# Optimization experiments

Measured on AMD Instinct MI355X. Metric: run time of the kernel, lower is better.

## Reference

```python
import jax, jax.numpy as jnp
import numpy as np

N_NODES = 50000
GRAPH_DIM = 256
QUERY_DIM = 256
BATCH = 512


def setup_inputs() -> dict:
    key = jax.random.key(0)
    k1, k2, k3 = jax.random.split(key, 3)
    graph_embs = jax.random.normal(k1, (N_NODES, GRAPH_DIM), dtype=jnp.float32)
    query_emb = jax.random.normal(k2, (BATCH, QUERY_DIM), dtype=jnp.float32)
    # nn.Linear(graph_dim + query_dim, 1): weight [1, G+Q] -> stored flat [G+Q], bias [1]
    attn_w = jax.random.normal(k3, (GRAPH_DIM + QUERY_DIM,), dtype=jnp.float32) * (1.0 / np.sqrt(GRAPH_DIM + QUERY_DIM))
    attn_b = jnp.zeros((1,), dtype=jnp.float32)
    return {"graph_embs": graph_embs, "query_emb": query_emb, "attn_w": attn_w, "attn_b": attn_b}


def reference(graph_embs, query_emb, attn_w, attn_b):
    # Linear on concat([graph, query]) == graph @ w_g + query @ w_q + b
    w_g = attn_w[:GRAPH_DIM]   # [G]
    w_q = attn_w[GRAPH_DIM:]   # [Q]
    g_score = graph_embs @ w_g            # [N]
    q_score = query_emb @ w_q             # [B]
    scores = q_score[:, None] + g_score[None, :] + attn_b[0]  # [B, N]
    attn_weights = jax.nn.softmax(scores, axis=-1)            # [B, N]
    pooled = attn_weights @ graph_embs                        # [B, G]
    return pooled
```

## Files before the change

### kernel.cpp

```cpp
#include <hip/hip_runtime.h>


#define N_NODES 50000
#define DIM     256
#define BATCH   512
#define CHUNK   50
#define GRID1   1000
#define NPART   8
#define POISON  0xAAAAAAAAu

__global__ __launch_bounds__(256) void qap_fused(
    const float* __restrict__ embs,
    const float* __restrict__ attn_w,
    float* __restrict__ part,
    float* __restrict__ zpart,
    unsigned int* __restrict__ counter,
    float* __restrict__ out)
{
    __shared__ float accLDS[4][DIM];
    __shared__ float zWave[4];
    __shared__ int   isLast;
    const int tid  = threadIdx.x;
    const int wave = tid >> 6;
    const int lane = tid & 63;
    const int beg  = blockIdx.x * CHUNK;
    const int rep  = blockIdx.x & (NPART - 1);

    const float4* emb4 = (const float4*)embs;
    const float4  w    = ((const float4*)attn_w)[lane];

    float4 acc  = {0.f, 0.f, 0.f, 0.f};
    float  zAcc = 0.f;

    for (int i = wave * 2; i < CHUNK; i += 8) {
        const float4 v0 = emb4[(size_t)(beg + i) * 64 + lane];
        const float4 v1 = emb4[(size_t)(beg + i + 1) * 64 + lane];
        float p0 = v0.x * w.x + v0.y * w.y + v0.z * w.z + v0.w * w.w;
        float p1 = v1.x * w.x + v1.y * w.y + v1.z * w.z + v1.w * w.w;
        #pragma unroll
        for (int off = 32; off >= 1; off >>= 1) {
            p0 += __shfl_xor(p0, off, 64);
            p1 += __shfl_xor(p1, off, 64);
        }
        const float e0 = __expf(p0);
        const float e1 = __expf(p1);
        zAcc += e0 + e1;
        acc.x = fmaf(e0, v0.x, fmaf(e1, v1.x, acc.x));
        acc.y = fmaf(e0, v0.y, fmaf(e1, v1.y, acc.y));
        acc.z = fmaf(e0, v0.z, fmaf(e1, v1.z, acc.z));
        acc.w = fmaf(e0, v0.w, fmaf(e1, v1.w, acc.w));
    }

    ((float4*)&accLDS[wave][0])[lane] = acc;
    if (lane == 0) zWave[wave] = zAcc;
    __syncthreads();
    const float s = accLDS[0][tid] + accLDS[1][tid] + accLDS[2][tid] + accLDS[3][tid];
    atomicAdd(&part[rep * DIM + tid], s);
    if (tid == 0)
        atomicAdd(&zpart[rep], zWave[0] + zWave[1] + zWave[2] + zWave[3]);

    __builtin_amdgcn_s_waitcnt(0);
    __syncthreads();
    if (tid == 0) {
        const unsigned int old = atomicAdd(counter, 1u);
        isLast = (old == POISON + (GRID1 - 1u)) || (old == GRID1 - 1u);
    }
    __syncthreads();
    if (!isLast) return;

    float sv = 0.f;
    #pragma unroll
    for (int j = 0; j < NPART; ++j)
        sv += __hip_atomic_load(&part[j * DIM + tid],
                                __ATOMIC_RELAXED, __HIP_MEMORY_SCOPE_AGENT);
    float z = 0.f;
    if (tid == 0) {
        #pragma unroll
        for (int j = 0; j < NPART; ++j)
            z += __hip_atomic_load(&zpart[j],
                                   __ATOMIC_RELAXED, __HIP_MEMORY_SCOPE_AGENT);
    }
    __shared__ float zsh;
    if (tid == 0) zsh = z;
    __shared__ float outv[DIM];
    __syncthreads();
    outv[tid] = sv * (1.0f / zsh);
    __syncthreads();

    const float4 o = ((const float4*)outv)[lane];
    float4* out4 = (float4*)out;
    for (int b = wave; b < BATCH; b += 4)
        out4[(size_t)b * 64 + lane] = o;
}

extern "C" void kernel_launch(void* const* d_in, const int* in_sizes, int n_in,
                              void* d_out, int out_size, void* d_ws, size_t ws_size,
                              hipStream_t stream) {
    const float* embs   = (const float*)d_in[0];
    const float* attn_w = (const float*)d_in[2];
    float* out = (float*)d_out;

    float*        part    = (float*)d_ws;
    float*        zpart   = part + NPART * DIM;
    unsigned int* counter = (unsigned int*)(zpart + NPART);

    qap_fused<<<GRID1, 256, 0, stream>>>(embs, attn_w, part, zpart, counter, out);
}
```

Measured before the change: 112.5 us.

## Spread final output broadcast across the last 512 finishing blocks

```diff
diff --git a/kernel.cpp b/kernel.cpp
--- a/kernel.cpp
+++ b/kernel.cpp
@@ -8,6 +8,7 @@
 #define GRID1   1000
 #define NPART   8
 #define POISON  0xAAAAAAAAu
+#define NWRITE  512
 
 __global__ __launch_bounds__(256) void qap_fused(
     const float* __restrict__ embs,
@@ -19,7 +20,7 @@
 {
     __shared__ float accLDS[4][DIM];
     __shared__ float zWave[4];
-    __shared__ int   isLast;
+    __shared__ unsigned int relTicket;
     const int tid  = threadIdx.x;
     const int wave = tid >> 6;
     const int lane = tid & 63;
@@ -63,34 +64,33 @@
     __syncthreads();
     if (tid == 0) {
         const unsigned int old = atomicAdd(counter, 1u);
-        isLast = (old == POISON + (GRID1 - 1u)) || (old == GRID1 - 1u);
+        relTicket = (old >= POISON) ? (old - POISON) : old;
     }
     __syncthreads();
-    if (!isLast) return;
+    const unsigned int rel = relTicket;
+    if (rel < GRID1 - NWRITE) return;
+    const int row = (int)(rel - (GRID1 - NWRITE));
 
-    float sv = 0.f;
+    if (tid == 0) {
+        for (;;) {
+            const unsigned int c = __hip_atomic_load(counter,
+                    __ATOMIC_RELAXED, __HIP_MEMORY_SCOPE_AGENT);
+            const unsigned int crel = (c >= POISON) ? (c - POISON) : c;
+            if (crel >= GRID1) break;
+            __builtin_amdgcn_s_sleep(2);
+        }
+    }
+    __syncthreads();
+
+    float sv = 0.f, z = 0.f;
     #pragma unroll
-    for (int j = 0; j < NPART; ++j)
+    for (int j = 0; j < NPART; ++j) {
         sv += __hip_atomic_load(&part[j * DIM + tid],
                                 __ATOMIC_RELAXED, __HIP_MEMORY_SCOPE_AGENT);
-    float z = 0.f;
-    if (tid == 0) {
-        #pragma unroll
-        for (int j = 0; j < NPART; ++j)
-            z += __hip_atomic_load(&zpart[j],
-                                   __ATOMIC_RELAXED, __HIP_MEMORY_SCOPE_AGENT);
+        z  += __hip_atomic_load(&zpart[j],
+                                __ATOMIC_RELAXED, __HIP_MEMORY_SCOPE_AGENT);
     }
-    __shared__ float zsh;
-    if (tid == 0) zsh = z;
-    __shared__ float outv[DIM];
-    __syncthreads();
-    outv[tid] = sv * (1.0f / zsh);
-    __syncthreads();
-
-    const float4 o = ((const float4*)outv)[lane];
-    float4* out4 = (float4*)out;
-    for (int b = wave; b < BATCH; b += 4)
-        out4[(size_t)b * 64 + lane] = o;
+    out[(size_t)row * DIM + tid] = sv * (1.0f / z);
 }
 
 extern "C" void kernel_launch(void* const* d_in, const int* in_sizes, int n_in,
```

New measurement: 131.3 us. +16.7%, slower.
